# Performance work log

Measured on AMD Instinct MI355X. Metric: run time of the kernel, lower is better.

Reference implementation:

```python
import jax, jax.numpy as jnp
import numpy as np

V, E, B, T = 50000, 512, 8, 512

def setup_inputs() -> dict:
    key = jax.random.key(0)
    ks = jax.random.split(key, 9)
    s_ih = 1.0 / np.sqrt(E)
    return {
        "x": jax.random.randint(ks[0], (B, T), 0, V, dtype=jnp.int64),
        "y": jax.random.randint(ks[1], (B, T), 0, V, dtype=jnp.int64),
        "embedding": jax.random.normal(ks[2], (V, E), dtype=jnp.float32),
        "w_ih": jax.random.uniform(ks[3], (4 * E, E), jnp.float32, -s_ih, s_ih),
        "w_hh": jax.random.uniform(ks[4], (4 * E, E), jnp.float32, -s_ih, s_ih),
        "b_ih": jax.random.uniform(ks[5], (4 * E,), jnp.float32, -s_ih, s_ih),
        "b_hh": jax.random.uniform(ks[6], (4 * E,), jnp.float32, -s_ih, s_ih),
        "dec_w": jax.random.uniform(ks[7], (V, E), jnp.float32, -s_ih, s_ih),
        "dec_b": jax.random.uniform(ks[8], (V,), jnp.float32, -s_ih, s_ih),
    }

def _lstm(embed, w_ih, w_hh, b_ih, b_hh):
    # embed: [B, T, E]. Precompute input projections for all timesteps.
    xproj = jnp.einsum("bte,ge->btg", embed, w_ih) + b_ih  # [B, T, 4E]
    xproj = jnp.swapaxes(xproj, 0, 1)                      # [T, B, 4E]
    h0 = jnp.zeros((embed.shape[0], w_hh.shape[1]), embed.dtype)
    c0 = jnp.zeros_like(h0)

    def step(carry, xp_t):
        h, c = carry
        gates = xp_t + h @ w_hh.T + b_hh          # [B, 4E]
        i, f, g, o = jnp.split(gates, 4, axis=-1)  # PyTorch gate order: i,f,g,o
        i = jax.nn.sigmoid(i)
        f = jax.nn.sigmoid(f)
        g = jnp.tanh(g)
        o = jax.nn.sigmoid(o)
        c = f * c + i * g
        h = o * jnp.tanh(c)
        return (h, c), h

    _, hs = jax.lax.scan(step, (h0, c0), xproj)   # hs: [T, B, E]
    return jnp.swapaxes(hs, 0, 1)                 # [B, T, E]

def reference(x, y, embedding, w_ih, w_hh, b_ih, b_hh, dec_w, dec_b):
    embed = embedding[x]                                   # [B, T, E]
    lstm_out = _lstm(embed, w_ih, w_hh, b_ih, b_hh)        # [B, T, E]
    y_pred = jnp.einsum("bte,ve->btv", lstm_out, dec_w) + dec_b  # [B, T, V]
    return y_pred
```

## Files before the change

kernel.cpp:

```cpp
#include <hip/hip_runtime.h>
#include <hip/hip_bf16.h>
#include <stdint.h>

typedef short bf16x8 __attribute__((ext_vector_type(8)));
typedef float f32x4 __attribute__((ext_vector_type(4)));

typedef const __attribute__((address_space(1))) unsigned int glob_u32;
typedef __attribute__((address_space(3))) unsigned int lds_u32;

__device__ __forceinline__ void gl_lds16(const void* g, void* s) {
  __builtin_amdgcn_global_load_lds((glob_u32*)g, (lds_u32*)s, 16, 0, 0);
}

__device__ __forceinline__ unsigned short f2bf(float f) {
  __hip_bfloat16 h = __float2bfloat16(f);
  return __builtin_bit_cast(unsigned short, h);
}
__device__ __forceinline__ float bf2f(unsigned short u) {
  __hip_bfloat16 h = __builtin_bit_cast(__hip_bfloat16, u);
  return __bfloat162float(h);
}

__device__ __forceinline__ float sigm_fast(float x) {
  float e = __expf(-x);
  return __builtin_amdgcn_rcpf(1.f + e);
}
__device__ __forceinline__ float tanh_fast(float x) {
  float e = __expf(2.f * x);
  return 1.f - 2.f * __builtin_amdgcn_rcpf(e + 1.f);
}

__global__ void split_hl(const float* __restrict__ src,
                         unsigned short* __restrict__ hi,
                         unsigned short* __restrict__ lo, int n4) {
  int i = blockIdx.x * blockDim.x + threadIdx.x;
  if (i >= n4) return;
  float4 v = reinterpret_cast<const float4*>(src)[i];
  ushort4 h, l;
  h.x = f2bf(v.x); l.x = f2bf(v.x - bf2f(h.x));
  h.y = f2bf(v.y); l.y = f2bf(v.y - bf2f(h.y));
  h.z = f2bf(v.z); l.z = f2bf(v.z - bf2f(h.z));
  h.w = f2bf(v.w); l.w = f2bf(v.w - bf2f(h.w));
  reinterpret_cast<ushort4*>(hi)[i] = h;
  reinterpret_cast<ushort4*>(lo)[i] = l;
}

__global__ void split_h(const float* __restrict__ src,
                        unsigned short* __restrict__ hi, int n4) {
  int i = blockIdx.x * blockDim.x + threadIdx.x;
  if (i >= n4) return;
  float4 v = reinterpret_cast<const float4*>(src)[i];
  ushort4 h;
  h.x = f2bf(v.x); h.y = f2bf(v.y); h.z = f2bf(v.z); h.w = f2bf(v.w);
  reinterpret_cast<ushort4*>(hi)[i] = h;
}

__global__ void gather_split(const int* __restrict__ x, const float* __restrict__ emb,
                             unsigned short* __restrict__ hi,
                             unsigned short* __restrict__ lo) {
  int i = blockIdx.x * 256 + threadIdx.x;
  int m = i >> 7, k4 = i & 127;
  long row = x[m];
  float4 v = reinterpret_cast<const float4*>(emb + row * 512)[k4];
  ushort4 h, l;
  h.x = f2bf(v.x); l.x = f2bf(v.x - bf2f(h.x));
  h.y = f2bf(v.y); l.y = f2bf(v.y - bf2f(h.y));
  h.z = f2bf(v.z); l.z = f2bf(v.z - bf2f(h.z));
  h.w = f2bf(v.w); l.w = f2bf(v.w - bf2f(h.w));
  reinterpret_cast<ushort4*>(hi)[m * 128 + k4] = h;
  reinterpret_cast<ushort4*>(lo)[m * 128 + k4] = l;
}

__global__ __launch_bounds__(256) void gemm_split(
    const unsigned short* __restrict__ Ahi, const unsigned short* __restrict__ Alo,
    const unsigned short* __restrict__ Bhi, const unsigned short* __restrict__ Blo,
    float* __restrict__ C, const float* __restrict__ bias1,
    const float* __restrict__ bias2, int N, int mtiles) {
  __shared__ unsigned short lds[4][128 * 64];
  int nwg = gridDim.x;
  int wid = (blockIdx.x & 7) * (nwg >> 3) + (blockIdx.x >> 3);
  int mt = wid % mtiles, nt = wid / mtiles;
  int m0 = mt * 128, n0 = nt * 128;
  int tid = threadIdx.x, l = tid & 63, w = tid >> 6;
  int wm = (w & 1) * 64, wn = (w >> 1) * 64;

  f32x4 acc[4][4];
#pragma unroll
  for (int a = 0; a < 4; ++a)
#pragma unroll
    for (int b = 0; b < 4; ++b) acc[a][b] = f32x4{0.f, 0.f, 0.f, 0.f};

  const unsigned short* srcs[4] = {Ahi, Alo, Bhi, Blo};

  for (int kc = 0; kc < 8; ++kc) {
    __syncthreads();
#pragma unroll
    for (int tile = 0; tile < 4; ++tile) {
      const unsigned short* src = srcs[tile];
      int rbase = (tile < 2) ? m0 : n0;
#pragma unroll
      for (int i = 0; i < 4; ++i) {
        int G = (i * 4 + w) * 64 + l;
        int r = G >> 3, g = G & 7;
        int row = rbase + r;
        long gb = (long)row * 1024 + kc * 128 + ((g * 16) ^ ((r & 7) << 4));
        gl_lds16((const char*)src + gb, (char*)(&lds[tile][0]) + (i * 4 + w) * 1024);
      }
    }
    __syncthreads();

    const char* ldsb = (const char*)&lds[0][0];
#pragma unroll
    for (int ks = 0; ks < 2; ++ks) {
      bf16x8 ah[4], al[4], bh[4], bl[4];
      int biw = ks * 64 + ((l >> 4) * 16);
#pragma unroll
      for (int fm = 0; fm < 4; ++fm) {
        int row = wm + fm * 16 + (l & 15);
        int off = row * 128 + (biw ^ ((row & 7) << 4));
        ah[fm] = *reinterpret_cast<const bf16x8*>(ldsb + off);
        al[fm] = *reinterpret_cast<const bf16x8*>(ldsb + 16384 + off);
      }
#pragma unroll
      for (int fn = 0; fn < 4; ++fn) {
        int row = wn + fn * 16 + (l & 15);
        int off = row * 128 + (biw ^ ((row & 7) << 4));
        bh[fn] = *reinterpret_cast<const bf16x8*>(ldsb + 32768 + off);
        bl[fn] = *reinterpret_cast<const bf16x8*>(ldsb + 49152 + off);
      }
#pragma unroll
      for (int fm = 0; fm < 4; ++fm)
#pragma unroll
        for (int fn = 0; fn < 4; ++fn) {
          acc[fm][fn] = __builtin_amdgcn_mfma_f32_16x16x32_bf16(ah[fm], bh[fn], acc[fm][fn], 0, 0, 0);
          acc[fm][fn] = __builtin_amdgcn_mfma_f32_16x16x32_bf16(ah[fm], bl[fn], acc[fm][fn], 0, 0, 0);
          acc[fm][fn] = __builtin_amdgcn_mfma_f32_16x16x32_bf16(al[fm], bh[fn], acc[fm][fn], 0, 0, 0);
        }
    }
  }

#pragma unroll
  for (int fn = 0; fn < 4; ++fn) {
    int n = n0 + wn + fn * 16 + (l & 15);
    float bs = bias1[n];
    if (bias2) bs += bias2[n];
#pragma unroll
    for (int fm = 0; fm < 4; ++fm) {
      int mb = m0 + wm + fm * 16 + (l >> 4) * 4;
#pragma unroll
      for (int j = 0; j < 4; ++j)
        C[(long)(mb + j) * N + n] = acc[fm][fn][j] + bs;
    }
  }
}

__global__ __launch_bounds__(256) void gemm_plain(
    const unsigned short* __restrict__ Ahi, const unsigned short* __restrict__ Bhi,
    float* __restrict__ C, const float* __restrict__ bias1, int N) {
  __shared__ unsigned short lds[2][128 * 64];
  int xcd = blockIdx.x & 7;
  int wid = blockIdx.x >> 3;
  int mt = xcd * 4 + (wid & 3);
  int nt = wid >> 2;
  int m0 = mt * 128, n0 = nt * 128;
  int tid = threadIdx.x, l = tid & 63, w = tid >> 6;
  int wm = (w & 1) * 64, wn = (w >> 1) * 64;

  f32x4 acc[4][4];
#pragma unroll
  for (int a = 0; a < 4; ++a)
#pragma unroll
    for (int b = 0; b < 4; ++b) acc[a][b] = f32x4{0.f, 0.f, 0.f, 0.f};

  const unsigned short* srcs[2] = {Ahi, Bhi};

  for (int kc = 0; kc < 8; ++kc) {
    __syncthreads();
#pragma unroll
    for (int tile = 0; tile < 2; ++tile) {
      const unsigned short* src = srcs[tile];
      int rbase = (tile < 1) ? m0 : n0;
#pragma unroll
      for (int i = 0; i < 4; ++i) {
        int G = (i * 4 + w) * 64 + l;
        int r = G >> 3, g = G & 7;
        int row = rbase + r;
        if (tile == 1 && row >= N) row = n0;
        long gb = (long)row * 1024 + kc * 128 + ((g * 16) ^ ((r & 7) << 4));
        gl_lds16((const char*)src + gb, (char*)(&lds[tile][0]) + (i * 4 + w) * 1024);
      }
    }
    __syncthreads();

    const char* ldsb = (const char*)&lds[0][0];
#pragma unroll
    for (int ks = 0; ks < 2; ++ks) {
      bf16x8 ah[4], bh[4];
      int biw = ks * 64 + ((l >> 4) * 16);
#pragma unroll
      for (int fm = 0; fm < 4; ++fm) {
        int row = wm + fm * 16 + (l & 15);
        int off = row * 128 + (biw ^ ((row & 7) << 4));
        ah[fm] = *reinterpret_cast<const bf16x8*>(ldsb + off);
      }
#pragma unroll
      for (int fn = 0; fn < 4; ++fn) {
        int row = wn + fn * 16 + (l & 15);
        int off = row * 128 + (biw ^ ((row & 7) << 4));
        bh[fn] = *reinterpret_cast<const bf16x8*>(ldsb + 16384 + off);
      }
#pragma unroll
      for (int fm = 0; fm < 4; ++fm)
#pragma unroll
        for (int fn = 0; fn < 4; ++fn)
          acc[fm][fn] = __builtin_amdgcn_mfma_f32_16x16x32_bf16(ah[fm], bh[fn], acc[fm][fn], 0, 0, 0);
    }
  }

#pragma unroll
  for (int fn = 0; fn < 4; ++fn) {
    int n = n0 + wn + fn * 16 + (l & 15);
    if (n < N) {
      float bs = bias1[n];
#pragma unroll
      for (int fm = 0; fm < 4; ++fm) {
        int mb = m0 + wm + fm * 16 + (l >> 4) * 4;
#pragma unroll
        for (int j = 0; j < 4; ++j)
          C[(long)(mb + j) * N + n] = acc[fm][fn][j] + bs;
      }
    }
  }
}

__global__ __launch_bounds__(256, 1) void lstm_persistent(
    const float* __restrict__ xproj,
    const float* __restrict__ whh,
    float* lstm_f32,
    unsigned short* __restrict__ lstm_hi) {
  int bid = blockIdx.x;
  int batch = bid & 7, slice = bid >> 3;
  int tid = threadIdx.x, l = tid & 63, w = tid >> 6;
  int g = l >> 4, e = l & 15;
  long R = (long)g * 512 + slice * 16 + e;

  __shared__ float h_s[512];
  __shared__ float part_s[2][4][64];

  float wr[128];
  {
    const float4* wp = reinterpret_cast<const float4*>(whh + R * 512) + w * 32;
#pragma unroll
    for (int jj = 0; jj < 32; ++jj) {
      float4 v = wp[jj];
      wr[jj * 4 + 0] = v.x; wr[jj * 4 + 1] = v.y;
      wr[jj * 4 + 2] = v.z; wr[jj * 4 + 3] = v.w;
    }
  }
#pragma unroll
  for (int jj = 0; jj < 128; jj += 4)
    asm volatile("" : "+v"(wr[jj]), "+v"(wr[jj + 1]), "+v"(wr[jj + 2]), "+v"(wr[jj + 3]));

  const float* xbase = xproj + (long)batch * 512 * 2048 + g * 512 + slice * 16 + e;
  float* hrow_base = lstm_f32 + (long)batch * 512 * 512;
  float c_reg = 0.f;

  for (int t = 0; t < 512; ++t) {
    float xp = 0.f;
    if (w == 0) xp = xbase[(long)t * 2048];

    float a0 = 0.f, a1 = 0.f, a2 = 0.f, a3 = 0.f;
    if (t > 0) {
      const unsigned long long* src = reinterpret_cast<const unsigned long long*>(
          hrow_base + (long)(t - 1) * 512 + w * 128) + l;
      unsigned long long u = __hip_atomic_load(src, __ATOMIC_RELAXED, __HIP_MEMORY_SCOPE_AGENT);
      unsigned long long u2 = __hip_atomic_load(src, __ATOMIC_RELAXED, __HIP_MEMORY_SCOPE_AGENT);
      while ((unsigned)u == 0xFFFFFFFFu || (unsigned)(u >> 32) == 0xFFFFFFFFu) {
        u = u2;
        u2 = __hip_atomic_load(src, __ATOMIC_RELAXED, __HIP_MEMORY_SCOPE_AGENT);
      }
      float2 hf;
      hf.x = __builtin_bit_cast(float, (unsigned)u);
      hf.y = __builtin_bit_cast(float, (unsigned)(u >> 32));
      *reinterpret_cast<float2*>(&h_s[w * 128 + 2 * l]) = hf;
      asm volatile("s_waitcnt lgkmcnt(0)" ::: "memory");
      __builtin_amdgcn_sched_barrier(0);
#pragma unroll
      for (int jj = 0; jj < 32; ++jj) {
        float4 h4 = *reinterpret_cast<const float4*>(&h_s[w * 128 + jj * 4]);
        a0 = fmaf(wr[jj * 4 + 0], h4.x, a0);
        a1 = fmaf(wr[jj * 4 + 1], h4.y, a1);
        a2 = fmaf(wr[jj * 4 + 2], h4.z, a2);
        a3 = fmaf(wr[jj * 4 + 3], h4.w, a3);
      }
    }
    part_s[t & 1][w][l] = (a0 + a1) + (a2 + a3);
    __syncthreads();

    if (w == 0) {
      float sum = xp + part_s[t & 1][0][l] + part_s[t & 1][1][l] +
                  part_s[t & 1][2][l] + part_s[t & 1][3][l];
      float val = (g == 2) ? tanh_fast(sum) : sigm_fast(sum);
      float vf = __shfl(val, e + 16);
      float vg = __shfl(val, e + 32);
      float vo = __shfl(val, e + 48);
      if (l < 16) {
        float c = vf * c_reg + val * vg;
        c_reg = c;
        float h = vo * tanh_fast(c);
        long oidx = ((long)batch * 512 + t) * 512 + slice * 16 + l;
        __hip_atomic_store(reinterpret_cast<unsigned int*>(lstm_f32) + oidx,
                           __builtin_bit_cast(unsigned int, h),
                           __ATOMIC_RELAXED, __HIP_MEMORY_SCOPE_AGENT);
        lstm_hi[oidx] = f2bf(h);
      }
    }
  }
}

extern "C" void kernel_launch(void* const* d_in, const int* in_sizes, int n_in,
                              void* d_out, int out_size, void* d_ws, size_t ws_size,
                              hipStream_t stream) {
  const int*   x         = (const int*)d_in[0];
  const float* embedding = (const float*)d_in[2];
  const float* w_ih      = (const float*)d_in[3];
  const float* w_hh      = (const float*)d_in[4];
  const float* b_ih      = (const float*)d_in[5];
  const float* b_hh      = (const float*)d_in[6];
  const float* dec_w     = (const float*)d_in[7];
  const float* dec_b     = (const float*)d_in[8];

  char* ws = (char*)d_ws;
  float* xproj = (float*)ws;                      ws += (size_t)4096 * 2048 * 4;
  float* lstmf = (float*)ws;                      ws += (size_t)4096 * 512 * 4;
  unsigned short* lstm_hi = (unsigned short*)ws;  ws += (size_t)4096 * 512 * 2;
  unsigned short* emb_hi  = (unsigned short*)ws;  ws += (size_t)4096 * 512 * 2;
  unsigned short* emb_lo  = (unsigned short*)ws;  ws += (size_t)4096 * 512 * 2;
  unsigned short* wih_hi  = (unsigned short*)ws;  ws += (size_t)2048 * 512 * 2;
  unsigned short* wih_lo  = (unsigned short*)ws;  ws += (size_t)2048 * 512 * 2;
  unsigned short* dw_hi   = (unsigned short*)ws;  ws += (size_t)50000 * 512 * 2;

  hipMemsetAsync(lstmf, 0xFF, (size_t)4096 * 512 * 4, stream);

  split_hl<<<1024, 256, 0, stream>>>(w_ih, wih_hi, wih_lo, 2048 * 512 / 4);
  split_h<<<25000, 256, 0, stream>>>(dec_w, dw_hi, 50000 * 512 / 4);
  gather_split<<<2048, 256, 0, stream>>>(x, embedding, emb_hi, emb_lo);

  gemm_split<<<32 * 16, 256, 0, stream>>>(emb_hi, emb_lo, wih_hi, wih_lo, xproj,
                                          b_ih, b_hh, 2048, 32);

  {
    void* args[] = {(void*)&xproj, (void*)&w_hh, (void*)&lstmf, (void*)&lstm_hi};
    hipLaunchCooperativeKernel((void*)lstm_persistent, dim3(256), dim3(256), args, 0, stream);
  }

  gemm_plain<<<32 * 391, 256, 0, stream>>>(lstm_hi, dw_hi, (float*)d_out, dec_b, 50000);
}
```

Measured before the change: 1.367 ms.

## Split LSTM recurrent dot product across eight waves per block

```diff
diff --git a/kernel.cpp b/kernel.cpp
--- a/kernel.cpp
+++ b/kernel.cpp
@@ -233,7 +233,7 @@
   }
 }
 
-__global__ __launch_bounds__(256, 1) void lstm_persistent(
+__global__ __launch_bounds__(512, 1) void lstm_persistent(
     const float* __restrict__ xproj,
     const float* __restrict__ whh,
     float* lstm_f32,
@@ -245,20 +245,20 @@
   long R = (long)g * 512 + slice * 16 + e;
 
   __shared__ float h_s[512];
-  __shared__ float part_s[2][4][64];
-
-  float wr[128];
+  __shared__ float part_s[2][64][9];
+
+  float wr[64];
   {
-    const float4* wp = reinterpret_cast<const float4*>(whh + R * 512) + w * 32;
-#pragma unroll
-    for (int jj = 0; jj < 32; ++jj) {
+    const float4* wp = reinterpret_cast<const float4*>(whh + R * 512 + w * 64);
+#pragma unroll
+    for (int jj = 0; jj < 16; ++jj) {
       float4 v = wp[jj];
       wr[jj * 4 + 0] = v.x; wr[jj * 4 + 1] = v.y;
       wr[jj * 4 + 2] = v.z; wr[jj * 4 + 3] = v.w;
     }
   }
 #pragma unroll
-  for (int jj = 0; jj < 128; jj += 4)
+  for (int jj = 0; jj < 64; jj += 4)
     asm volatile("" : "+v"(wr[jj]), "+v"(wr[jj + 1]), "+v"(wr[jj + 2]), "+v"(wr[jj + 3]));
 
   const float* xbase = xproj + (long)batch * 512 * 2048 + g * 512 + slice * 16 + e;
@@ -271,35 +271,32 @@
 
     float a0 = 0.f, a1 = 0.f, a2 = 0.f, a3 = 0.f;
     if (t > 0) {
-      const unsigned long long* src = reinterpret_cast<const unsigned long long*>(
-          hrow_base + (long)(t - 1) * 512 + w * 128) + l;
-      unsigned long long u = __hip_atomic_load(src, __ATOMIC_RELAXED, __HIP_MEMORY_SCOPE_AGENT);
-      unsigned long long u2 = __hip_atomic_load(src, __ATOMIC_RELAXED, __HIP_MEMORY_SCOPE_AGENT);
-      while ((unsigned)u == 0xFFFFFFFFu || (unsigned)(u >> 32) == 0xFFFFFFFFu) {
-        u = u2;
-        u2 = __hip_atomic_load(src, __ATOMIC_RELAXED, __HIP_MEMORY_SCOPE_AGENT);
-      }
-      float2 hf;
-      hf.x = __builtin_bit_cast(float, (unsigned)u);
-      hf.y = __builtin_bit_cast(float, (unsigned)(u >> 32));
-      *reinterpret_cast<float2*>(&h_s[w * 128 + 2 * l]) = hf;
+      const unsigned int* src = reinterpret_cast<const unsigned int*>(
+          hrow_base + (long)(t - 1) * 512 + w * 64 + l);
+#define PLOAD() __hip_atomic_load(src, __ATOMIC_RELAXED, __HIP_MEMORY_SCOPE_AGENT)
+      unsigned p0 = PLOAD(), p1 = PLOAD(), p2 = PLOAD(), p3 = PLOAD();
+      while (p0 == 0xFFFFFFFFu) { p0 = p1; p1 = p2; p2 = p3; p3 = PLOAD(); }
+#undef PLOAD
+      h_s[w * 64 + l] = __builtin_bit_cast(float, p0);
       asm volatile("s_waitcnt lgkmcnt(0)" ::: "memory");
       __builtin_amdgcn_sched_barrier(0);
-#pragma unroll
-      for (int jj = 0; jj < 32; ++jj) {
-        float4 h4 = *reinterpret_cast<const float4*>(&h_s[w * 128 + jj * 4]);
+      const float4* hv = reinterpret_cast<const float4*>(&h_s[w * 64]);
+#pragma unroll
+      for (int jj = 0; jj < 16; ++jj) {
+        float4 h4 = hv[jj];
         a0 = fmaf(wr[jj * 4 + 0], h4.x, a0);
         a1 = fmaf(wr[jj * 4 + 1], h4.y, a1);
         a2 = fmaf(wr[jj * 4 + 2], h4.z, a2);
         a3 = fmaf(wr[jj * 4 + 3], h4.w, a3);
       }
     }
-    part_s[t & 1][w][l] = (a0 + a1) + (a2 + a3);
+    part_s[t & 1][l][w] = (a0 + a1) + (a2 + a3);
     __syncthreads();
 
     if (w == 0) {
-      float sum = xp + part_s[t & 1][0][l] + part_s[t & 1][1][l] +
-                  part_s[t & 1][2][l] + part_s[t & 1][3][l];
+      const float* pr = &part_s[t & 1][l][0];
+      float sum = xp + ((pr[0] + pr[1]) + (pr[2] + pr[3])) +
+                  ((pr[4] + pr[5]) + (pr[6] + pr[7]));
       float val = (g == 2) ? tanh_fast(sum) : sigm_fast(sum);
       float vf = __shfl(val, e + 16);
       float vg = __shfl(val, e + 32);
@@ -351,7 +348,7 @@
 
   {
     void* args[] = {(void*)&xproj, (void*)&w_hh, (void*)&lstmf, (void*)&lstm_hi};
-    hipLaunchCooperativeKernel((void*)lstm_persistent, dim3(256), dim3(256), args, 0, stream);
+    hipLaunchCooperativeKernel((void*)lstm_persistent, dim3(256), dim3(512), args, 0, stream);
   }
 
   gemm_plain<<<32 * 391, 256, 0, stream>>>(lstm_hi, dw_hi, (float*)d_out, dec_b, 50000);
```

Result: slower. 1.494 ms (+9.3%).

## Broadcast h via readlane instead of LDS, prefetch xproj, deepen poll pipeline

Applied to the files above, without the earlier changes.

```diff
diff --git a/kernel.cpp b/kernel.cpp
--- a/kernel.cpp
+++ b/kernel.cpp
@@ -28,6 +28,11 @@
 __device__ __forceinline__ float tanh_fast(float x) {
   float e = __expf(2.f * x);
   return 1.f - 2.f * __builtin_amdgcn_rcpf(e + 1.f);
+}
+
+__device__ __forceinline__ float readl(float v, int lane) {
+  return __builtin_bit_cast(float,
+      __builtin_amdgcn_readlane(__builtin_bit_cast(int, v), lane));
 }
 
 __global__ void split_hl(const float* __restrict__ src,
@@ -244,12 +249,11 @@
   int g = l >> 4, e = l & 15;
   long R = (long)g * 512 + slice * 16 + e;
 
-  __shared__ float h_s[512];
   __shared__ float part_s[2][4][64];
 
   float wr[128];
   {
-    const float4* wp = reinterpret_cast<const float4*>(whh + R * 512) + w * 32;
+    const float4* wp = reinterpret_cast<const float4*>(whh + R * 512 + w * 128);
 #pragma unroll
     for (int jj = 0; jj < 32; ++jj) {
       float4 v = wp[jj];
@@ -265,41 +269,38 @@
   float* hrow_base = lstm_f32 + (long)batch * 512 * 512;
   float c_reg = 0.f;
 
+  float xp_cur = 0.f, xp_nxt = 0.f;
+  if (w == 0) xp_cur = xbase[0];
+
   for (int t = 0; t < 512; ++t) {
-    float xp = 0.f;
-    if (w == 0) xp = xbase[(long)t * 2048];
+    if (w == 0 && t < 511) xp_nxt = xbase[(long)(t + 1) * 2048];
 
     float a0 = 0.f, a1 = 0.f, a2 = 0.f, a3 = 0.f;
     if (t > 0) {
       const unsigned long long* src = reinterpret_cast<const unsigned long long*>(
           hrow_base + (long)(t - 1) * 512 + w * 128) + l;
-      unsigned long long u = __hip_atomic_load(src, __ATOMIC_RELAXED, __HIP_MEMORY_SCOPE_AGENT);
-      unsigned long long u2 = __hip_atomic_load(src, __ATOMIC_RELAXED, __HIP_MEMORY_SCOPE_AGENT);
-      while ((unsigned)u == 0xFFFFFFFFu || (unsigned)(u >> 32) == 0xFFFFFFFFu) {
-        u = u2;
-        u2 = __hip_atomic_load(src, __ATOMIC_RELAXED, __HIP_MEMORY_SCOPE_AGENT);
-      }
-      float2 hf;
-      hf.x = __builtin_bit_cast(float, (unsigned)u);
-      hf.y = __builtin_bit_cast(float, (unsigned)(u >> 32));
-      *reinterpret_cast<float2*>(&h_s[w * 128 + 2 * l]) = hf;
-      asm volatile("s_waitcnt lgkmcnt(0)" ::: "memory");
-      __builtin_amdgcn_sched_barrier(0);
-#pragma unroll
-      for (int jj = 0; jj < 32; ++jj) {
-        float4 h4 = *reinterpret_cast<const float4*>(&h_s[w * 128 + jj * 4]);
-        a0 = fmaf(wr[jj * 4 + 0], h4.x, a0);
-        a1 = fmaf(wr[jj * 4 + 1], h4.y, a1);
-        a2 = fmaf(wr[jj * 4 + 2], h4.z, a2);
-        a3 = fmaf(wr[jj * 4 + 3], h4.w, a3);
-      }
-    }
-    part_s[t & 1][w][l] = (a0 + a1) + (a2 + a3);
+#define PLOAD() __hip_atomic_load(src, __ATOMIC_RELAXED, __HIP_MEMORY_SCOPE_AGENT)
+      unsigned long long p0 = PLOAD(), p1 = PLOAD(), p2 = PLOAD(), p3 = PLOAD();
+      while ((unsigned)p0 == 0xFFFFFFFFu || (unsigned)(p0 >> 32) == 0xFFFFFFFFu) {
+        p0 = p1; p1 = p2; p2 = p3; p3 = PLOAD();
+      }
+#undef PLOAD
+      float hlo = __builtin_bit_cast(float, (unsigned)p0);
+      float hhi = __builtin_bit_cast(float, (unsigned)(p0 >> 32));
+#pragma unroll
+      for (int j = 0; j < 64; ++j) {
+        float hx = readl(hlo, j);
+        float hy = readl(hhi, j);
+        a0 = fmaf(wr[2 * j], hx, a0);
+        a1 = fmaf(wr[2 * j + 1], hy, a1);
+      }
+    }
+    part_s[t & 1][w][l] = a0 + a1 + (a2 + a3);
     __syncthreads();
 
     if (w == 0) {
-      float sum = xp + part_s[t & 1][0][l] + part_s[t & 1][1][l] +
-                  part_s[t & 1][2][l] + part_s[t & 1][3][l];
+      float sum = xp_cur + (part_s[t & 1][0][l] + part_s[t & 1][1][l]) +
+                  (part_s[t & 1][2][l] + part_s[t & 1][3][l]);
       float val = (g == 2) ? tanh_fast(sum) : sigm_fast(sum);
       float vf = __shfl(val, e + 16);
       float vg = __shfl(val, e + 32);
@@ -314,6 +315,7 @@
                            __ATOMIC_RELAXED, __HIP_MEMORY_SCOPE_AGENT);
         lstm_hi[oidx] = f2bf(h);
       }
+      xp_cur = xp_nxt;
     }
   }
 }
```

Result: slower. 1.458 ms (+6.7%).
